# Optimization experiments

Measured on AMD Instinct MI355X. Metric: run time of the kernel, lower is better.

The kernel has to match this reference:

```python
import jax, jax.numpy as jnp
import numpy as np

HID = 2048
HEADS = 16
HEAD = HID // HEADS  # 128
INTER = 8192
EPS = 1e-5
THETA = 10000.0
B, S = 2, 2048


def _layernorm(x, scale, bias):
    mu = jnp.mean(x, axis=-1, keepdims=True)
    var = jnp.var(x, axis=-1, keepdims=True)
    return (x - mu) * jax.lax.rsqrt(var + EPS) * scale + bias


def _rope(x, cos, sin):
    # x: [b,s,h,d]; adjacent pairs form complex numbers (per apply_rotary_emb)
    xr = x.reshape(*x.shape[:-1], HEAD // 2, 2)
    x0, x1 = xr[..., 0], xr[..., 1]
    o0 = x0 * cos - x1 * sin
    o1 = x0 * sin + x1 * cos
    return jnp.stack((o0, o1), axis=-1).reshape(x.shape)


def setup_inputs() -> dict:
    key = jax.random.key(0)
    ks = jax.random.split(key, 6)
    sc = 0.02
    return {
        "hidden_states": jax.random.normal(ks[0], (B, S, HID), jnp.float32),
        "attention_mask": jnp.zeros((B, 1, 1, S), jnp.float32),
        "w_qkv": (jax.random.normal(ks[1], (HID, 3 * HID), jnp.float32) * sc),
        "b_qkv": jnp.zeros((3 * HID,), jnp.float32),
        "w_o": (jax.random.normal(ks[2], (HID, HID), jnp.float32) * sc),
        "b_o": jnp.zeros((HID,), jnp.float32),
        "ln1_scale": jnp.ones((HID,), jnp.float32),
        "ln1_bias": jnp.zeros((HID,), jnp.float32),
        "ln2_scale": jnp.ones((HID,), jnp.float32),
        "ln2_bias": jnp.zeros((HID,), jnp.float32),
        "w_in": (jax.random.normal(ks[3], (HID, INTER), jnp.float32) * sc),
        "b_in": jnp.zeros((INTER,), jnp.float32),
        "w_out": (jax.random.normal(ks[4], (INTER, HID), jnp.float32) * sc),
        "b_out": jnp.zeros((HID,), jnp.float32),
    }


def reference(hidden_states, attention_mask, w_qkv, b_qkv, w_o, b_o,
              ln1_scale, ln1_bias, ln2_scale, ln2_bias,
              w_in, b_in, w_out, b_out):
    b, s, d = hidden_states.shape
    # ---- attention branch ----
    x1 = _layernorm(hidden_states, ln1_scale, ln1_bias)
    qkv = x1 @ w_qkv + b_qkv
    q, k, v = jnp.split(qkv, 3, axis=-1)
    q = q.reshape(b, s, HEADS, HEAD)
    k = k.reshape(b, s, HEADS, HEAD)
    v = v.reshape(b, s, HEADS, HEAD)
    # rotary embedding (complex pairing of adjacent elements)
    inv_freq = 1.0 / (THETA ** (jnp.arange(0, HEAD, 2, dtype=jnp.float32) / HEAD))
    freqs = jnp.arange(s, dtype=jnp.float32)[:, None] * inv_freq[None, :]  # [s, HEAD/2]
    cos = jnp.cos(freqs)[None, :, None, :]
    sin = jnp.sin(freqs)[None, :, None, :]
    q = _rope(q, cos, sin)
    k = _rope(k, cos, sin)
    # NOTE: source multiplies by sqrt(head_size) (faithful to original code)
    factor = jnp.sqrt(jnp.float32(HEAD))
    attn = jnp.einsum('bqhd,bkhd->bhqk', q, k) * factor  # [b,h,s,s]
    causal = jnp.tril(jnp.ones((s, s), dtype=bool))
    bias = jnp.where(causal, 0.0, jnp.finfo(jnp.float32).min)
    attn = attn + bias[None, None, :, :] + attention_mask
    p = jax.nn.softmax(attn, axis=-1)
    ao = jnp.einsum('bhqk,bkhd->bqhd', p, v).reshape(b, s, d)
    attn_out = ao @ w_o + b_o
    # ---- mlp branch (parallel residual) ----
    x2 = _layernorm(hidden_states, ln2_scale, ln2_bias)
    mlp = jax.nn.gelu(x2 @ w_in + b_in, approximate=False) @ w_out + b_out
    return mlp + hidden_states + attn_out
```

## Files before the change

### kernel.cpp

```cpp
#include <hip/hip_runtime.h>
#include <math.h>

#define HID 2048
#define NH 16
#define HD 128
#define INTER 8192
#define BB 2
#define SS 2048
#define MT (BB*SS)

typedef __bf16 bf16x8 __attribute__((ext_vector_type(8)));
typedef _Float16 f16x8 __attribute__((ext_vector_type(8)));
typedef float f32x4 __attribute__((ext_vector_type(4)));
typedef unsigned short u16x8 __attribute__((ext_vector_type(8)));

__device__ __forceinline__ float bf2f(unsigned short u) {
  unsigned v = ((unsigned)u) << 16;
  return __builtin_bit_cast(float, v);
}
__device__ __forceinline__ unsigned short f2bf(float x) {
  unsigned u = __builtin_bit_cast(unsigned, x);
  u += 0x7fffu + ((u >> 16) & 1u);
  return (unsigned short)(u >> 16);
}
__device__ __forceinline__ unsigned short f2h(float x) {
  _Float16 h = (_Float16)x;
  return __builtin_bit_cast(unsigned short, h);
}
__device__ __forceinline__ void gll16(const void* g, const void* lds) {
  __builtin_amdgcn_global_load_lds(
      (const __attribute__((address_space(1))) void*)g,
      (__attribute__((address_space(3))) void*)lds, 16, 0, 0);
}

__global__ __launch_bounds__(256) void ln2k(
    const float* __restrict__ X, const float* __restrict__ s1,
    const float* __restrict__ b1, const float* __restrict__ s2,
    const float* __restrict__ b2, unsigned short* __restrict__ X1f,
    unsigned short* __restrict__ X2) {
  const int row = blockIdx.x;
  const int tid = threadIdx.x;
  const float* x = X + (long)row * HID;
  float4 v0 = ((const float4*)x)[tid * 2];
  float4 v1 = ((const float4*)x)[tid * 2 + 1];
  float s = v0.x + v0.y + v0.z + v0.w + v1.x + v1.y + v1.z + v1.w;
  float q = v0.x * v0.x + v0.y * v0.y + v0.z * v0.z + v0.w * v0.w +
            v1.x * v1.x + v1.y * v1.y + v1.z * v1.z + v1.w * v1.w;
#pragma unroll
  for (int off = 1; off < 64; off <<= 1) {
    s += __shfl_xor(s, off);
    q += __shfl_xor(q, off);
  }
  __shared__ float rs[4], rq[4];
  const int wid = tid >> 6, lane = tid & 63;
  if (lane == 0) { rs[wid] = s; rq[wid] = q; }
  __syncthreads();
  s = rs[0] + rs[1] + rs[2] + rs[3];
  q = rq[0] + rq[1] + rq[2] + rq[3];
  const float mu = s * (1.f / HID);
  const float var = q * (1.f / HID) - mu * mu;
  const float rstd = rsqrtf(var + 1e-5f);
  float xv[8] = {v0.x, v0.y, v0.z, v0.w, v1.x, v1.y, v1.z, v1.w};
  u16x8 o1, o2;
#pragma unroll
  for (int e = 0; e < 8; e++) {
    const int j = tid * 8 + e;
    const float xn = (xv[e] - mu) * rstd;
    o1[e] = f2h(xn * s1[j] + b1[j]);
    o2[e] = f2bf(xn * s2[j] + b2[j]);
  }
  *(u16x8*)(X1f + (long)row * HID + tid * 8) = o1;
  *(u16x8*)(X2 + (long)row * HID + tid * 8) = o2;
}

template <bool F16>
__global__ __launch_bounds__(256) void wtrans(const float* __restrict__ W,
                                              unsigned short* __restrict__ WT,
                                              int K, int N, int ldn, int coff) {
  (void)N;
  __shared__ float t[32][33];
  const int n0 = blockIdx.x * 32, k0 = blockIdx.y * 32;
  const int tx = threadIdx.x, ty = threadIdx.y;
#pragma unroll
  for (int r = 0; r < 4; r++)
    t[ty + r * 8][tx] = W[(long)(k0 + ty + r * 8) * ldn + coff + n0 + tx];
  __syncthreads();
#pragma unroll
  for (int r = 0; r < 4; r++) {
    const float v = t[tx][ty + r * 8];
    WT[(long)(n0 + ty + r * 8) * K + k0 + tx] = F16 ? f2h(v) : f2bf(v);
  }
}

__global__ void rope_tab(float2* __restrict__ rope) {
  const int s = blockIdx.x, i = threadIdx.x;
  const double ang = (double)s * pow(10000.0, -(double)i / 64.0);
  rope[s * 64 + i] = make_float2((float)cos(ang), (float)sin(ang));
}

template <int MODE, bool F16>
__global__ __launch_bounds__(512) void gemm256(
    const unsigned short* __restrict__ A, const unsigned short* __restrict__ Bt,
    const float* __restrict__ bias, void* __restrict__ Cout, int N, int K,
    const float2* __restrict__ rope, unsigned short* __restrict__ QF,
    unsigned short* __restrict__ KF, unsigned short* __restrict__ Vb,
    float* __restrict__ P1) {
  __shared__ unsigned short As[2][256 * 64];
  __shared__ unsigned short Bs[2][256 * 64];
  const int tid = threadIdx.x;
  const int wid = tid >> 6, lane = tid & 63;
  const int l16 = lane & 15, lhi = lane >> 4;
  const int wr = wid >> 2, wc = wid & 3;
  const long rA0 = (long)blockIdx.y * 256;
  const long rB0 = (long)blockIdx.x * 256;
  const int nkt = (MODE == 4) ? (K / 128) : (K / 64);
  const int k0 = (MODE == 4) ? (int)blockIdx.z * (K / 2) : 0;

  f32x4 acc[8][4] = {};

  auto stage = [&](int kt2, int bu) {
#pragma unroll
    for (int i = 0; i < 4; i++) {
      const int lin = i * 8192 + tid * 16;
      const int row = lin >> 7;
      const int cs = ((lin >> 4) & 7) ^ (row & 7);
      const int dst = i * 8192 + wid * 1024;
      const long g = k0 + kt2 * 64 + cs * 8;
      gll16(A + (rA0 + row) * (long)K + g, (const char*)As[bu] + dst);
      gll16(Bt + (rB0 + row) * (long)K + g, (const char*)Bs[bu] + dst);
    }
  };

  stage(0, 0);
  asm volatile("s_waitcnt vmcnt(0)" ::: "memory");
  __builtin_amdgcn_s_barrier();
  int buf = 0;
  for (int kt = 0; kt < nkt; kt++) {
    u16x8 bv[4];
#pragma unroll
    for (int q = 0; q < 4; q++) {
      const int ks = q >> 1, mh = q & 1;
      if (q == 0 && kt + 1 < nkt) stage(kt + 1, buf ^ 1);
      if (mh == 0) {
#pragma unroll
        for (int n = 0; n < 4; n++) {
          const int row = wc * 64 + n * 16 + l16;
          const int ch = (ks * 4 + lhi) ^ (row & 7);
          bv[n] = *(const u16x8*)((const char*)Bs[buf] + row * 128 + ch * 16);
        }
      }
      u16x8 av[4];
#pragma unroll
      for (int m = 0; m < 4; m++) {
        const int row = wr * 128 + (mh * 4 + m) * 16 + l16;
        const int ch = (ks * 4 + lhi) ^ (row & 7);
        av[m] = *(const u16x8*)((const char*)As[buf] + row * 128 + ch * 16);
      }
      __builtin_amdgcn_s_barrier();
      __builtin_amdgcn_s_setprio(1);
#pragma unroll
      for (int m = 0; m < 4; m++)
#pragma unroll
        for (int n = 0; n < 4; n++) {
          if constexpr (F16)
            acc[mh * 4 + m][n] = __builtin_amdgcn_mfma_f32_16x16x32_f16(
                __builtin_bit_cast(f16x8, av[m]),
                __builtin_bit_cast(f16x8, bv[n]), acc[mh * 4 + m][n], 0, 0, 0);
          else
            acc[mh * 4 + m][n] = __builtin_amdgcn_mfma_f32_16x16x32_bf16(
                __builtin_bit_cast(bf16x8, av[m]),
                __builtin_bit_cast(bf16x8, bv[n]), acc[mh * 4 + m][n], 0, 0, 0);
        }
      __builtin_amdgcn_s_setprio(0);
      if (q == 3 && kt + 1 < nkt) {
        asm volatile("s_waitcnt vmcnt(0)" ::: "memory");
        __builtin_amdgcn_sched_barrier(0);
      }
      __builtin_amdgcn_s_barrier();
    }
    buf ^= 1;
  }

  const int b_ = (int)(rA0 >> 11);
#pragma unroll
  for (int m = 0; m < 8; m++) {
#pragma unroll
    for (int n = 0; n < 4; n++) {
      const int col = (int)rB0 + wc * 64 + n * 16 + l16;
      const float bsv = (MODE == 4) ? 0.f : bias[col];
      const int cq = col & 2047;
      const int i = (cq & 127) >> 1;
      const int hh = (cq >> 7) & 15;
      const int d = cq & 127;
#pragma unroll
      for (int r = 0; r < 4; r++) {
        const long row = rA0 + wr * 128 + m * 16 + lhi * 4 + r;
        float v = acc[m][n][r] + bsv;
        if (MODE == 1) {
          v = 0.5f * v * (1.f + erff(v * 0.7071067811865475f));
          ((unsigned short*)Cout)[row * N + col] = f2bf(v);
        } else if (MODE == 4) {
          float* dst = blockIdx.z ? P1 : (float*)Cout;
          dst[row * N + col] = v;
        } else if (MODE == 3) {
          const int srow = (int)row & 2047;
          if (col < 4096) {
            const float p = __shfl_xor(v, 1);
            const float2 cs = rope[srow * 64 + i];
            const float o = ((lane & 1) == 0) ? (v * cs.x - p * cs.y)
                                              : (p * cs.y + v * cs.x);
            unsigned short* dst = (col < 2048) ? QF : KF;
            dst[((long)(b_ * NH + hh) * SS + srow) * HD + d] = f2h(o);
          } else {
            Vb[row * HID + (col - 4096)] = f2bf(v);
          }
        }
      }
    }
  }
}

__global__ __launch_bounds__(256) void mlpfin(
    const float* __restrict__ P0, const float* __restrict__ P1,
    const float* __restrict__ bias, const float* __restrict__ hidden,
    const unsigned short* __restrict__ ATT, float* __restrict__ out) {
  const long i = ((long)blockIdx.x * 256 + threadIdx.x) * 4;
  float4 a = *(const float4*)(P0 + i);
  float4 b = *(const float4*)(P1 + i);
  float4 hc = *(const float4*)(hidden + i);
  ushort4 t = *(const ushort4*)(ATT + i);
  float4 bs = *(const float4*)(bias + (int)(i & 2047));
  float4 o;
  o.x = a.x + b.x + bs.x + hc.x + bf2f(t.x);
  o.y = a.y + b.y + bs.y + hc.y + bf2f(t.y);
  o.z = a.z + b.z + bs.z + hc.z + bf2f(t.z);
  o.w = a.w + b.w + bs.w + hc.w + bf2f(t.w);
  *(float4*)(out + i) = o;
}

__global__ __launch_bounds__(256) void vtrans(
    const unsigned short* __restrict__ Vb, unsigned short* __restrict__ VTb) {
  __shared__ unsigned short t[32][33];
  const int bh = blockIdx.z, b = bh >> 4, h = bh & 15;
  const int d0 = blockIdx.x * 32, s0 = blockIdx.y * 32;
  const int tx = threadIdx.x, ty = threadIdx.y;
#pragma unroll
  for (int r = 0; r < 4; r++) {
    const int s = s0 + ty + r * 8;
    t[ty + r * 8][tx] = Vb[((long)(b * SS + s)) * HID + h * HD + d0 + tx];
  }
  __syncthreads();
#pragma unroll
  for (int r = 0; r < 4; r++) {
    const int d = d0 + ty + r * 8;
    VTb[((long)bh * HD + d) * SS + s0 + tx] = t[tx][ty + r * 8];
  }
}

template <int MODE>
__global__ __launch_bounds__(256) void gemm128(
    const unsigned short* __restrict__ A, const unsigned short* __restrict__ Bt,
    const float* __restrict__ bias, void* __restrict__ Cout, int M, int N,
    int K, const float* __restrict__ residF,
    const unsigned short* __restrict__ residB) {
  (void)M;
  __shared__ unsigned short As[128 * 64];
  __shared__ unsigned short Bs[128 * 64];
  const int tid = threadIdx.x;
  const int wid = tid >> 6, lane = tid & 63;
  const int l16 = lane & 15, lhi = lane >> 4;
  const int bn = blockIdx.x, bm = blockIdx.y;
  const int wr = wid >> 1, wc = wid & 1;
  const long rA0 = (long)bm * 128;
  const long rB0 = (long)bn * 128;

  f32x4 acc[4][4] = {};

  for (int kt = 0; kt < K; kt += 64) {
#pragma unroll
    for (int i = 0; i < 4; i++) {
      const int lin = i * 4096 + wid * 1024 + (lane << 4);
      const int row = lin >> 7;
      const int cs = ((lin >> 4) & 7) ^ (row & 7);
      gll16(A + (rA0 + row) * (long)K + kt + cs * 8,
            (const char*)As + (i * 4096 + wid * 1024));
      gll16(Bt + (rB0 + row) * (long)K + kt + cs * 8,
            (const char*)Bs + (i * 4096 + wid * 1024));
    }
    __syncthreads();
#pragma unroll
    for (int ks = 0; ks < 2; ks++) {
      bf16x8 av[4], bv[4];
#pragma unroll
      for (int m = 0; m < 4; m++) {
        const int row = wr * 64 + m * 16 + l16;
        const int ch = (ks * 4 + lhi) ^ (row & 7);
        av[m] = *(const bf16x8*)((const char*)As + row * 128 + ch * 16);
      }
#pragma unroll
      for (int n = 0; n < 4; n++) {
        const int row = wc * 64 + n * 16 + l16;
        const int ch = (ks * 4 + lhi) ^ (row & 7);
        bv[n] = *(const bf16x8*)((const char*)Bs + row * 128 + ch * 16);
      }
#pragma unroll
      for (int m = 0; m < 4; m++)
#pragma unroll
        for (int n = 0; n < 4; n++)
          acc[m][n] = __builtin_amdgcn_mfma_f32_16x16x32_bf16(av[m], bv[n],
                                                              acc[m][n], 0, 0, 0);
    }
    __syncthreads();
  }

#pragma unroll
  for (int m = 0; m < 4; m++) {
#pragma unroll
    for (int n = 0; n < 4; n++) {
      const long col = rB0 + wc * 64 + n * 16 + l16;
      const float bsv = bias[col];
#pragma unroll
      for (int r = 0; r < 4; r++) {
        const long row = rA0 + wr * 64 + m * 16 + lhi * 4 + r;
        float v = acc[m][n][r] + bsv;
        if (MODE == 1) v = 0.5f * v * (1.f + erff(v * 0.7071067811865475f));
        if (MODE == 2) {
          v += residF[row * N + col] + bf2f(residB[row * N + col]);
          ((float*)Cout)[row * N + col] = v;
        } else {
          ((unsigned short*)Cout)[row * N + col] = f2bf(v);
        }
      }
    }
  }
}

__global__ __launch_bounds__(512, 2) void flash(
    const unsigned short* __restrict__ QF, const unsigned short* __restrict__ KF,
    const unsigned short* __restrict__ VT, const float* __restrict__ amask,
    unsigned short* __restrict__ AO) {
  __shared__ unsigned short Kt[2][64 * 128];
  __shared__ unsigned short Vt[2][128 * 64];
  __shared__ unsigned short Pl[8 * 1024];
  __shared__ float maskL[SS];
  const int z = blockIdx.x;
  const int qt = 15 - (z >> 5);
  const int bh = z & 31;
  const int b = bh >> 4, h = bh & 15;
  const int tid = threadIdx.x, wid = tid >> 6, lane = tid & 63;
  const int l16 = lane & 15, lhi = lane >> 4;
  const unsigned short* Qfb = QF + (long)bh * SS * HD;
  const unsigned short* Kfb = KF + (long)bh * SS * HD;
  const unsigned short* Vb = VT + (long)bh * HD * SS;
  const int q0 = qt * 128 + wid * 16;
  const float LOG2E = 1.4426950408889634f;
  const float SCL2 = 16.322232154552f;

  {
    float4 m0 = ((const float4*)(amask + (long)b * SS))[tid];
    m0.x *= LOG2E; m0.y *= LOG2E; m0.z *= LOG2E; m0.w *= LOG2E;
    ((float4*)maskL)[tid] = m0;
  }

  f16x8 qf[4];
#pragma unroll
  for (int ks = 0; ks < 4; ks++)
    qf[ks] = *(const f16x8*)(Qfb + (long)(q0 + l16) * HD + ks * 32 + lhi * 8);

  auto stage = [&](int kt2, int bu) {
#pragma unroll
    for (int i = 0; i < 2; i++) {
      const int lin = i * 8192 + wid * 1024 + (lane << 4);
      const int dst = i * 8192 + wid * 1024;
      {
        const int row = lin >> 8;
        const int cs = ((lin >> 4) & 15) ^ (row & 7);
        gll16(Kfb + (long)(kt2 * 64 + row) * HD + cs * 8,
              (const char*)Kt[bu] + dst);
      }
      {
        const int row = lin >> 7;
        const int cs = ((lin >> 4) & 7) ^ (row & 7);
        gll16(Vb + (long)row * SS + kt2 * 64 + cs * 8, (const char*)Vt[bu] + dst);
      }
    }
  };

  f32x4 accO[8] = {};
  float mrow[4], lrow[4];
#pragma unroll
  for (int r = 0; r < 4; r++) { mrow[r] = -3e38f; lrow[r] = 0.f; }

  const int nkt = 2 * qt + 2;
  stage(0, 0);
  asm volatile("s_waitcnt lgkmcnt(0)" ::: "memory");
  int buf = 0;
  for (int kt = 0; kt < nkt; kt++) {
    if (kt + 1 < nkt) {
      stage(kt + 1, buf ^ 1);
      asm volatile("s_waitcnt vmcnt(4)" ::: "memory");
    } else {
      asm volatile("s_waitcnt vmcnt(0)" ::: "memory");
    }
    __builtin_amdgcn_s_barrier();

    const bool active = (kt * 64 <= q0 + 15);
    if (active) {
      f32x4 accS[4] = {};
      __builtin_amdgcn_s_setprio(1);
#pragma unroll
      for (int ks = 0; ks < 4; ks++) {
        f16x8 bk[4];
#pragma unroll
        for (int nf = 0; nf < 4; nf++) {
          const int row = nf * 16 + l16;
          const int ch = (ks * 4 + lhi) ^ (row & 7);
          bk[nf] = *(const f16x8*)((const char*)Kt[buf] + row * 256 + ch * 16);
        }
#pragma unroll
        for (int nf = 0; nf < 4; nf++)
          accS[nf] = __builtin_amdgcn_mfma_f32_16x16x32_f16(qf[ks], bk[nf],
                                                            accS[nf], 0, 0, 0);
      }
      __builtin_amdgcn_s_setprio(0);

      float mk[4];
#pragma unroll
      for (int nf = 0; nf < 4; nf++) mk[nf] = maskL[kt * 64 + nf * 16 + l16];
#pragma unroll
      for (int nf = 0; nf < 4; nf++)
#pragma unroll
        for (int r = 0; r < 4; r++) {
          const int key = kt * 64 + nf * 16 + l16;
          const int qg = q0 + lhi * 4 + r;
          const float sv = accS[nf][r] * SCL2 + mk[nf];
          accS[nf][r] = (key > qg) ? -1e30f : sv;
        }

      float mx[4];
#pragma unroll
      for (int r = 0; r < 4; r++) {
        float m0 = fmaxf(fmaxf(accS[0][r], accS[1][r]),
                         fmaxf(accS[2][r], accS[3][r]));
        m0 = fmaxf(m0, __shfl_xor(m0, 1));
        m0 = fmaxf(m0, __shfl_xor(m0, 2));
        m0 = fmaxf(m0, __shfl_xor(m0, 4));
        m0 = fmaxf(m0, __shfl_xor(m0, 8));
        mx[r] = m0;
      }
      bool defer = true;
#pragma unroll
      for (int r = 0; r < 4; r++) defer = defer && (mx[r] <= mrow[r] + 8.f);
      if (!__all(defer)) {
#pragma unroll
        for (int r = 0; r < 4; r++) {
          const float mnew = fmaxf(mrow[r], mx[r]);
          const float alpha = exp2f(mrow[r] - mnew);
          mrow[r] = mnew;
          lrow[r] *= alpha;
#pragma unroll
          for (int nf2 = 0; nf2 < 8; nf2++) accO[nf2][r] *= alpha;
        }
      }
#pragma unroll
      for (int r = 0; r < 4; r++) {
        const int rowl = lhi * 4 + r;
        const int qg = q0 + rowl;
        float rsum = 0.f;
#pragma unroll
        for (int nf = 0; nf < 4; nf++) {
          const int key = kt * 64 + nf * 16 + l16;
          const float p = (key > qg) ? 0.f : exp2f(accS[nf][r] - mrow[r]);
          rsum += p;
          const int colv = nf * 16 + l16;
          const int slot = (colv >> 3) ^ (rowl & 7);
          *(unsigned short*)((char*)Pl + wid * 2048 + rowl * 128 + slot * 16 +
                             (colv & 7) * 2) = f2bf(p);
        }
        rsum += __shfl_xor(rsum, 1);
        rsum += __shfl_xor(rsum, 2);
        rsum += __shfl_xor(rsum, 4);
        rsum += __shfl_xor(rsum, 8);
        lrow[r] += rsum;
      }

      __builtin_amdgcn_s_setprio(1);
#pragma unroll
      for (int ks2 = 0; ks2 < 2; ks2++) {
        const int chp = (ks2 * 4 + lhi) ^ (l16 & 7);
        bf16x8 pa =
            *(const bf16x8*)((const char*)Pl + wid * 2048 + l16 * 128 + chp * 16);
#pragma unroll
        for (int nf2 = 0; nf2 < 8; nf2++) {
          const int rowv = nf2 * 16 + l16;
          const int ch = (ks2 * 4 + lhi) ^ (rowv & 7);
          bf16x8 vv =
              *(const bf16x8*)((const char*)Vt[buf] + rowv * 128 + ch * 16);
          accO[nf2] = __builtin_amdgcn_mfma_f32_16x16x32_bf16(pa, vv,
                                                              accO[nf2], 0, 0, 0);
        }
      }
      __builtin_amdgcn_s_setprio(0);
    }
    __builtin_amdgcn_s_barrier();
    buf ^= 1;
  }

#pragma unroll
  for (int nf2 = 0; nf2 < 8; nf2++)
#pragma unroll
    for (int r = 0; r < 4; r++) {
      const int qg = q0 + lhi * 4 + r;
      const int d = nf2 * 16 + l16;
      const float v = accO[nf2][r] / lrow[r];
      AO[((long)(b * SS + qg)) * HID + h * HD + d] = f2bf(v);
    }
}

extern "C" void kernel_launch(void* const* d_in, const int* in_sizes, int n_in,
                              void* d_out, int out_size, void* d_ws,
                              size_t ws_size, hipStream_t stream) {
  (void)in_sizes; (void)n_in; (void)out_size;
  const float* hidden = (const float*)d_in[0];
  const float* amask = (const float*)d_in[1];
  const float* w_qkv = (const float*)d_in[2];
  const float* b_qkv = (const float*)d_in[3];
  const float* w_o = (const float*)d_in[4];
  const float* b_o = (const float*)d_in[5];
  const float* ln1s = (const float*)d_in[6];
  const float* ln1b = (const float*)d_in[7];
  const float* ln2s = (const float*)d_in[8];
  const float* ln2b = (const float*)d_in[9];
  const float* w_in = (const float*)d_in[10];
  const float* b_in = (const float*)d_in[11];
  const float* w_out = (const float*)d_in[12];
  const float* b_out = (const float*)d_in[13];

  char* ws = (char*)d_ws;
  unsigned short* X1f = (unsigned short*)(ws + 0);
  unsigned short* X2  = (unsigned short*)(ws + 16777216);
  unsigned short* Vbf = (unsigned short*)(ws + 33554432);
  unsigned short* WQ  = (unsigned short*)(ws + 50331648);
  unsigned short* QFb = (unsigned short*)(ws + 75497472);
  unsigned short* KFb = (unsigned short*)(ws + 92274688);
  unsigned short* VTb = (unsigned short*)(ws + 109051904);
  unsigned short* ATT = (unsigned short*)(ws + 125829120);
  unsigned short* WD  = (unsigned short*)(ws + 142606336);
  float2* ROPE = (float2*)(ws + 176160768);
  float* P1 = (float*)(ws + 177209344);
  if (ws_size < 210763776) return;

  unsigned short* AO = X1f;
  unsigned short* H1 = WQ;
  float* P0 = (float*)ws;

  ln2k<<<MT, 256, 0, stream>>>(hidden, ln1s, ln1b, ln2s, ln2b, X1f, X2);
  rope_tab<<<SS, 64, 0, stream>>>(ROPE);
  wtrans<true><<<dim3(192, 64), dim3(32, 8), 0, stream>>>(w_qkv, WQ, HID,
                                                          3 * HID, 3 * HID, 0);
  gemm256<3, true><<<dim3(24, 16), 512, 0, stream>>>(
      X1f, WQ, b_qkv, nullptr, 3 * HID, HID, ROPE, QFb, KFb, Vbf, nullptr);
  vtrans<<<dim3(4, 64, 32), dim3(32, 8), 0, stream>>>(Vbf, VTb);
  flash<<<512, 512, 0, stream>>>(QFb, KFb, VTb, amask, AO);
  wtrans<false><<<dim3(64, 64), dim3(32, 8), 0, stream>>>(w_o, WD, HID, HID,
                                                          HID, 0);
  gemm128<0><<<dim3(16, 32), 256, 0, stream>>>(AO, WD, b_o, ATT, MT, HID, HID,
                                               nullptr, nullptr);
  wtrans<false><<<dim3(256, 64), dim3(32, 8), 0, stream>>>(w_in, WD, HID,
                                                           INTER, INTER, 0);
  gemm256<1, false><<<dim3(32, 16), 512, 0, stream>>>(
      X2, WD, b_in, H1, INTER, HID, nullptr, nullptr, nullptr, nullptr, nullptr);
  wtrans<false><<<dim3(64, 256), dim3(32, 8), 0, stream>>>(w_out, WD, INTER,
                                                           HID, HID, 0);
  gemm256<4, false><<<dim3(8, 16, 2), 512, 0, stream>>>(
      H1, WD, nullptr, P0, HID, INTER, nullptr, nullptr, nullptr, nullptr, P1);
  mlpfin<<<8192, 256, 0, stream>>>(P0, P1, b_out, hidden, ATT, (float*)d_out);
}
```

Baseline: 825.2 us.

## Switch GEMM main loop to 4-stage K32 pipeline with partial vmcnt waits

Replaces the double-buffered K=64 LDS staging with a four-slot ring of K=32 tiles, prefetching three tiles ahead and using counted vmcnt waits instead of a full drain each iteration. The LDS swizzle is changed to suit 64-byte rows. The goal is to hide global-load latency behind the MFMAs and drop the blocking vmcnt(0) barrier. In exchange there are more iterations and barriers per K, and the swizzle may cause more LDS bank conflicts. Correctness depends on the hand-set vmcnt counts matching four loads per stage and on the barrier placement that protects ring slots from being overwritten while still in use.

```diff
diff --git a/kernel.cpp b/kernel.cpp
--- a/kernel.cpp
+++ b/kernel.cpp
@@ -105,58 +105,69 @@
     const float2* __restrict__ rope, unsigned short* __restrict__ QF,
     unsigned short* __restrict__ KF, unsigned short* __restrict__ Vb,
     float* __restrict__ P1) {
-  __shared__ unsigned short As[2][256 * 64];
-  __shared__ unsigned short Bs[2][256 * 64];
+  __shared__ unsigned short As[4][256 * 32];
+  __shared__ unsigned short Bs[4][256 * 32];
   const int tid = threadIdx.x;
   const int wid = tid >> 6, lane = tid & 63;
   const int l16 = lane & 15, lhi = lane >> 4;
   const int wr = wid >> 2, wc = wid & 3;
   const long rA0 = (long)blockIdx.y * 256;
   const long rB0 = (long)blockIdx.x * 256;
-  const int nkt = (MODE == 4) ? (K / 128) : (K / 64);
+  const int KK = (MODE == 4) ? (K / 2) : K;
   const int k0 = (MODE == 4) ? (int)blockIdx.z * (K / 2) : 0;
+  const int nkt = KK / 32;
 
   f32x4 acc[8][4] = {};
 
-  auto stage = [&](int kt2, int bu) {
-#pragma unroll
-    for (int i = 0; i < 4; i++) {
-      const int lin = i * 8192 + tid * 16;
-      const int row = lin >> 7;
-      const int cs = ((lin >> 4) & 7) ^ (row & 7);
+  auto stage = [&](int kt2) {
+    const int sl = kt2 & 3;
+#pragma unroll
+    for (int i = 0; i < 2; i++) {
+      const int d = i * 8192 + tid * 16;
+      const int row = d >> 6;
+      const int ch = ((d >> 4) & 3) ^ ((row >> 1) & 3);
       const int dst = i * 8192 + wid * 1024;
-      const long g = k0 + kt2 * 64 + cs * 8;
-      gll16(A + (rA0 + row) * (long)K + g, (const char*)As[bu] + dst);
-      gll16(Bt + (rB0 + row) * (long)K + g, (const char*)Bs[bu] + dst);
+      const long g = k0 + kt2 * 32 + ch * 8;
+      gll16(A + (rA0 + row) * (long)K + g, (const char*)As[sl] + dst);
+      gll16(Bt + (rB0 + row) * (long)K + g, (const char*)Bs[sl] + dst);
     }
   };
 
-  stage(0, 0);
-  asm volatile("s_waitcnt vmcnt(0)" ::: "memory");
-  __builtin_amdgcn_s_barrier();
-  int buf = 0;
+  stage(0);
+  stage(1);
+  stage(2);
   for (int kt = 0; kt < nkt; kt++) {
+    const int sl = kt & 3;
+    if (kt + 3 < nkt) {
+      stage(kt + 3);
+      asm volatile("s_waitcnt vmcnt(12)" ::: "memory");
+    } else if (kt + 2 < nkt) {
+      asm volatile("s_waitcnt vmcnt(8)" ::: "memory");
+    } else if (kt + 1 < nkt) {
+      asm volatile("s_waitcnt vmcnt(4)" ::: "memory");
+    } else {
+      asm volatile("s_waitcnt vmcnt(0)" ::: "memory");
+    }
+    __builtin_amdgcn_s_barrier();
+
     u16x8 bv[4];
 #pragma unroll
-    for (int q = 0; q < 4; q++) {
-      const int ks = q >> 1, mh = q & 1;
-      if (q == 0 && kt + 1 < nkt) stage(kt + 1, buf ^ 1);
+    for (int mh = 0; mh < 2; mh++) {
       if (mh == 0) {
 #pragma unroll
         for (int n = 0; n < 4; n++) {
           const int row = wc * 64 + n * 16 + l16;
-          const int ch = (ks * 4 + lhi) ^ (row & 7);
-          bv[n] = *(const u16x8*)((const char*)Bs[buf] + row * 128 + ch * 16);
+          const int ch = lhi ^ ((row >> 1) & 3);
+          bv[n] = *(const u16x8*)((const char*)Bs[sl] + row * 64 + ch * 16);
         }
       }
       u16x8 av[4];
 #pragma unroll
       for (int m = 0; m < 4; m++) {
-        const int row = wr * 128 + (mh * 4 + m) * 16 + l16;
-        const int ch = (ks * 4 + lhi) ^ (row & 7);
-        av[m] = *(const u16x8*)((const char*)As[buf] + row * 128 + ch * 16);
-      }
-      __builtin_amdgcn_s_barrier();
+        const int row = wr * 128 + mh * 64 + m * 16 + l16;
+        const int ch = lhi ^ ((row >> 1) & 3);
+        av[m] = *(const u16x8*)((const char*)As[sl] + row * 64 + ch * 16);
+      }
       __builtin_amdgcn_s_setprio(1);
 #pragma unroll
       for (int m = 0; m < 4; m++)
@@ -172,13 +183,8 @@
                 __builtin_bit_cast(bf16x8, bv[n]), acc[mh * 4 + m][n], 0, 0, 0);
         }
       __builtin_amdgcn_s_setprio(0);
-      if (q == 3 && kt + 1 < nkt) {
-        asm volatile("s_waitcnt vmcnt(0)" ::: "memory");
-        __builtin_amdgcn_sched_barrier(0);
-      }
       __builtin_amdgcn_s_barrier();
     }
-    buf ^= 1;
   }
 
   const int b_ = (int)(rA0 >> 11);
```

After: 841.0 us. No clear change (+1.9%).
